# Kernel optimization log

Hardware: AMD Instinct MI355X
Metric: run time of the kernel (lower is better)

## Reference

```python
import jax, jax.numpy as jnp
import numpy as np

B, S, D, H = 2, 2048, 1024, 16
DK = D // H
NEG = -1.0e9


def setup_inputs() -> dict:
    key = jax.random.key(0)
    ks = jax.random.split(key, 11)
    inp = {
        "q": jax.random.normal(ks[0], (B, S, D), jnp.float32),
        "k": jax.random.normal(ks[1], (B, S, D), jnp.float32),
        "v": jax.random.normal(ks[2], (B, S, D), jnp.float32),
        "mask": jnp.tril(jnp.ones((S, S), jnp.int32))[None, None],  # causal [1,1,S,S]
    }
    scale = 0.02
    inp["w_q"] = jax.random.normal(ks[3], (D, D), jnp.float32) * scale
    inp["b_q"] = jnp.zeros((D,), jnp.float32)
    inp["w_k"] = jax.random.normal(ks[4], (D, D), jnp.float32) * scale
    inp["b_k"] = jnp.zeros((D,), jnp.float32)
    inp["w_v"] = jax.random.normal(ks[5], (D, D), jnp.float32) * scale
    inp["b_v"] = jnp.zeros((D,), jnp.float32)
    inp["w_o"] = jax.random.normal(ks[6], (D, D), jnp.float32) * scale
    inp["b_o"] = jnp.zeros((D,), jnp.float32)
    return inp


def reference(q, k, v, mask, w_q, b_q, w_k, b_k, w_v, b_v, w_o, b_o):
    # projections: [B,S,D] -> [B,H,S,DK]
    def proj(x, w, b):
        y = jnp.einsum("bsd,de->bse", x, w) + b
        return y.reshape(B, S, H, DK).transpose(0, 2, 1, 3)

    Q = proj(q, w_q, b_q)
    K = proj(k, w_k, b_k)
    V = proj(v, w_v, b_v)
    # explicit scores matrix, faithful to the original naive attention
    scores = jnp.einsum("bhsd,bhtd->bhst", Q, K) / jnp.sqrt(jnp.float32(DK))
    scores = jnp.where(mask == 0, NEG, scores)
    attn = jax.nn.softmax(scores, axis=-1)  # dropout p=0.0 -> identity
    x = jnp.einsum("bhst,bhtd->bhsd", attn, V)
    x = x.transpose(0, 2, 1, 3).reshape(B, S, D)
    return jnp.einsum("bsd,de->bse", x, w_o) + b_o
```

## Files before the change

kernel.cpp:

```cpp
#include <hip/hip_runtime.h>
#include <hip/hip_bf16.h>

typedef __bf16 bf16;
typedef __bf16 bf16x2 __attribute__((ext_vector_type(2)));
typedef __bf16 bf16x8 __attribute__((ext_vector_type(8)));
typedef float f32x4 __attribute__((ext_vector_type(4)));

#define MFMA16(a, b, c) __builtin_amdgcn_mfma_f32_16x16x32_bf16(a, b, c, 0, 0, 0)

#define QSCALE 0.18033688f

#define GLOAD_LDS(g, l)                                              \
  __builtin_amdgcn_global_load_lds(                                  \
      (const __attribute__((address_space(1))) void*)(g),            \
      (__attribute__((address_space(3))) void*)(l), 16, 0, 0)

__global__ __launch_bounds__(256) void convert_k(const float* __restrict__ q,
                                                 const float* __restrict__ k,
                                                 const float* __restrict__ v,
                                                 bf16* __restrict__ qb,
                                                 bf16* __restrict__ kb,
                                                 bf16* __restrict__ vb) {
  const float* src = blockIdx.y == 0 ? q : blockIdx.y == 1 ? k : v;
  bf16* dst = blockIdx.y == 0 ? qb : blockIdx.y == 1 ? kb : vb;
  const size_t i = ((size_t)blockIdx.x * 256 + threadIdx.x) * 8;
  float4 a = *(const float4*)(src + i);
  float4 b = *(const float4*)(src + i + 4);
  bf16x8 o;
  o[0] = (bf16)a.x; o[1] = (bf16)a.y; o[2] = (bf16)a.z; o[3] = (bf16)a.w;
  o[4] = (bf16)b.x; o[5] = (bf16)b.y; o[6] = (bf16)b.z; o[7] = (bf16)b.w;
  *(bf16x8*)(dst + i) = o;
}

__global__ __launch_bounds__(256) void transpose_w(const float* __restrict__ w0,
                                                   const float* __restrict__ w1,
                                                   const float* __restrict__ w2,
                                                   const float* __restrict__ w3,
                                                   bf16* __restrict__ dst) {
  __shared__ bf16 T[64][68];
  const float* W = blockIdx.z == 0 ? w0 : blockIdx.z == 1 ? w1
                   : blockIdx.z == 2 ? w2 : w3;
  bf16* Y = dst + (size_t)blockIdx.z * 1024 * 1024;
  const int t = threadIdx.x, r = t >> 2, c4 = t & 3;
  const int k0 = blockIdx.y * 64, n0 = blockIdx.x * 64;

  const float4* src = (const float4*)(W + (size_t)(k0 + r) * 1024 + n0 + c4 * 16);
  float4 f0 = src[0], f1 = src[1], f2 = src[2], f3 = src[3];
  bf16* row = &T[r][c4 * 16];
  row[0] = (bf16)f0.x; row[1] = (bf16)f0.y; row[2] = (bf16)f0.z; row[3] = (bf16)f0.w;
  row[4] = (bf16)f1.x; row[5] = (bf16)f1.y; row[6] = (bf16)f1.z; row[7] = (bf16)f1.w;
  row[8] = (bf16)f2.x; row[9] = (bf16)f2.y; row[10] = (bf16)f2.z; row[11] = (bf16)f2.w;
  row[12] = (bf16)f3.x; row[13] = (bf16)f3.y; row[14] = (bf16)f3.z; row[15] = (bf16)f3.w;
  __syncthreads();

  bf16x8 o0, o1;
#pragma unroll
  for (int j = 0; j < 8; ++j) o0[j] = T[c4 * 16 + j][r];
#pragma unroll
  for (int j = 0; j < 8; ++j) o1[j] = T[c4 * 16 + 8 + j][r];
  bf16* d = Y + (size_t)(n0 + r) * 1024 + k0 + c4 * 16;
  *(bf16x8*)d = o0;
  *(bf16x8*)(d + 8) = o1;
}

template <int QKV, int MT>
__global__ __launch_bounds__(256) void gemm128(
    const bf16* __restrict__ xq, const bf16* __restrict__ xk,
    const bf16* __restrict__ xv, const bf16* __restrict__ Wt,
    const float* __restrict__ bq, const float* __restrict__ bk,
    const float* __restrict__ bv, bf16* __restrict__ Qp,
    bf16* __restrict__ Kp, bf16* __restrict__ Vtp, float* __restrict__ Yf) {
  __shared__ bf16 Al[MT * 32 * 32];
  __shared__ bf16 Bl[128 * 32];

  const int z = QKV ? blockIdx.z : 0;
  const bf16* X = QKV ? (z == 0 ? xq : z == 1 ? xk : xv) : xq;
  const bf16* Bt = Wt + (size_t)z * 1048576;
  const float* bias = QKV ? (z == 0 ? bq : z == 1 ? bk : bv) : bq;
  const float escale = (QKV && z == 0) ? QSCALE : 1.0f;

  const int t = threadIdx.x;
  const int wave = t >> 6, lane = t & 63, quad = lane >> 4, l16 = lane & 15;
  const int wm = (wave >> 1) * (MT * 16), wn = (wave & 1) * 64;
  const int bm = blockIdx.y * (MT * 32), bn = blockIdx.x * 128;

  const int off = wave * 1024 + lane * 16;
  const int srow = off >> 6;
  const int scol = (off & 63) >> 1;
  const bf16* gA0 = X + (size_t)(bm + srow) * 1024 + scol;
  const bf16* gA1 = X + (size_t)(bm + 64 + srow) * 1024 + scol;
  const bf16* gB0 = Bt + (size_t)(bn + srow) * 1024 + scol;
  const bf16* gB1 = Bt + (size_t)(bn + 64 + srow) * 1024 + scol;
  bf16* ldsA0 = Al + wave * 512;
  bf16* ldsA1 = Al + 2048 + wave * 512;
  bf16* ldsB0 = Bl + wave * 512;
  bf16* ldsB1 = Bl + 2048 + wave * 512;

  f32x4 acc[MT][4] = {};

  for (int kb = 0; kb < 1024; kb += 32) {
    GLOAD_LDS(gA0 + kb, ldsA0);
    if (MT == 4) GLOAD_LDS(gA1 + kb, ldsA1);
    GLOAD_LDS(gB0 + kb, ldsB0);
    GLOAD_LDS(gB1 + kb, ldsB1);
    __syncthreads();

    bf16x8 af[MT], bfr[4];
#pragma unroll
    for (int mt = 0; mt < MT; ++mt)
      af[mt] = *(const bf16x8*)(Al + (wm + mt * 16 + l16) * 32 + quad * 8);
#pragma unroll
    for (int nt = 0; nt < 4; ++nt)
      bfr[nt] = *(const bf16x8*)(Bl + (wn + nt * 16 + l16) * 32 + quad * 8);
#pragma unroll
    for (int mt = 0; mt < MT; ++mt)
#pragma unroll
      for (int nt = 0; nt < 4; ++nt)
        acc[mt][nt] = MFMA16(af[mt], bfr[nt], acc[mt][nt]);
    __syncthreads();
  }

  if (QKV && z == 2) {
    __shared__ bf16 Tt[64 * 136];
    const int b = bm >> 11;
#pragma unroll
    for (int half = 0; half < 2; ++half) {
      if ((wave & 1) == half) {
#pragma unroll
        for (int nt = 0; nt < 4; ++nt) {
          const int ln = nt * 16 + l16;
          const float bia = bias[bn + half * 64 + ln];
#pragma unroll
          for (int mt = 0; mt < 4; ++mt)
#pragma unroll
            for (int r = 0; r < 4; ++r) {
              const int m = wm + mt * 16 + quad * 4 + r;
              Tt[ln * 136 + m] = (bf16)(acc[mt][nt][r] + bia);
            }
        }
      }
      __syncthreads();
      {
        const int ln = t >> 2, seg = (t & 3) * 32;
        const int gn = bn + half * 64 + ln;
        const int h = gn >> 6, dk = gn & 63;
        const int s0 = (bm & 2047) + seg;
        bf16* dst = Vtp + ((size_t)(b * 16 + h) * 64 + dk) * 2048 + s0;
        const bf16* srcp = Tt + ln * 136 + seg;
#pragma unroll
        for (int j = 0; j < 4; ++j)
          *(bf16x8*)(dst + j * 8) = *(const bf16x8*)(srcp + j * 8);
      }
      __syncthreads();
    }
  } else {
#pragma unroll
    for (int mt = 0; mt < MT; ++mt)
#pragma unroll
      for (int nt = 0; nt < 4; ++nt) {
        const int gn = bn + wn + nt * 16 + l16;
        const float bia = bias[gn];
#pragma unroll
        for (int r = 0; r < 4; ++r) {
          const int gm = bm + wm + mt * 16 + quad * 4 + r;
          const float val = (acc[mt][nt][r] + bia) * escale;
          if (!QKV) {
            Yf[(size_t)gm * 1024 + gn] = val;
          } else {
            const int b = gm >> 11, s = gm & 2047;
            const int h = gn >> 6, dk = gn & 63;
            bf16* Y = (z == 0) ? Qp : Kp;
            Y[((size_t)(b * 16 + h) * 2048 + s) * 64 + dk] = (bf16)val;
          }
        }
      }
  }
}

__global__ __launch_bounds__(256) void attn_k(const bf16* __restrict__ Q,
                                              const bf16* __restrict__ K,
                                              const bf16* __restrict__ Vt,
                                              bf16* __restrict__ X) {
  __shared__ bf16 Kl[64 * 72];
  __shared__ bf16 Vl[64 * 72];
  __shared__ bf16 Pb[4][16 * 72];

  const int t = threadIdx.x;
  const int wave = t >> 6, lane = t & 63, quad = lane >> 4, l16 = lane & 15;
  const int pairx = blockIdx.x, bh = blockIdx.y;
  const int b = bh >> 4, h = bh & 15;

  const bf16* Qb = Q + (size_t)bh * 2048 * 64;
  const bf16* Kb = K + (size_t)bh * 2048 * 64;
  const bf16* Vb = Vt + (size_t)bh * 64 * 2048;

  const int srow = t >> 2;
  const int scol = (t & 3) * 16;

  bf16x8 onesf;
#pragma unroll
  for (int i = 0; i < 8; ++i) onesf[i] = (bf16)1.0f;

  bf16* Pw = Pb[wave];

  for (int phase = 0; phase < 2; ++phase) {
    const int qtile = phase ? (31 - pairx) : pairx;
    const int ntiles = qtile + 1;
    const int q0 = qtile * 64 + wave * 16;

    bf16x8 qf0 = *(const bf16x8*)(Qb + (q0 + l16) * 64 + quad * 8);
    bf16x8 qf1 = *(const bf16x8*)(Qb + (q0 + l16) * 64 + 32 + quad * 8);

    f32x4 o[4] = {};
    f32x4 o4 = {};

    {
      const bf16* kp = Kb + srow * 64 + scol;
      const bf16* vp = Vb + (size_t)srow * 2048 + scol;
      bf16x8 k0r = *(const bf16x8*)kp;
      bf16x8 k1r = *(const bf16x8*)(kp + 8);
      bf16x8 v0r = *(const bf16x8*)vp;
      bf16x8 v1r = *(const bf16x8*)(vp + 8);
      *(bf16x8*)(Kl + srow * 72 + scol) = k0r;
      *(bf16x8*)(Kl + srow * 72 + scol + 8) = k1r;
      *(bf16x8*)(Vl + srow * 72 + scol) = v0r;
      *(bf16x8*)(Vl + srow * 72 + scol + 8) = v1r;
    }
    __syncthreads();

    for (int kt = 0; kt < ntiles; ++kt) {
      const int k0 = kt * 64;
      const bool more = (kt + 1) < ntiles;
      bf16x8 kr0, kr1, vr0, vr1;
      if (more) {
        const bf16* kp = Kb + (k0 + 64 + srow) * 64 + scol;
        const bf16* vp = Vb + (size_t)srow * 2048 + k0 + 64 + scol;
        kr0 = *(const bf16x8*)kp;
        kr1 = *(const bf16x8*)(kp + 8);
        vr0 = *(const bf16x8*)vp;
        vr1 = *(const bf16x8*)(vp + 8);
      }

      f32x4 sc[4];
#pragma unroll
      for (int nt = 0; nt < 4; ++nt) {
        bf16x8 kf0 = *(const bf16x8*)(Kl + (nt * 16 + l16) * 72 + quad * 8);
        bf16x8 kf1 = *(const bf16x8*)(Kl + (nt * 16 + l16) * 72 + 32 + quad * 8);
        f32x4 s = {};
        s = MFMA16(qf0, kf0, s);
        s = MFMA16(qf1, kf1, s);
        sc[nt] = s;
      }

#pragma unroll
      for (int r = 0; r < 4; ++r) {
        const int row = quad * 4 + r;
        const int qg = q0 + row;
#pragma unroll
        for (int nt = 0; nt < 4; ++nt) {
          const int key = k0 + nt * 16 + l16;
          const float p = (key <= qg) ? exp2f(sc[nt][r]) : 0.f;
          Pw[row * 72 + nt * 16 + l16] = (bf16)p;
        }
      }
      __builtin_amdgcn_s_waitcnt(0xC07F);

      bf16x8 pf0 = *(const bf16x8*)(Pw + l16 * 72 + quad * 8);
      bf16x8 pf1 = *(const bf16x8*)(Pw + l16 * 72 + 32 + quad * 8);
      o4 = MFMA16(pf0, onesf, o4);
      o4 = MFMA16(pf1, onesf, o4);
#pragma unroll
      for (int dt = 0; dt < 4; ++dt) {
        bf16x8 vf0 = *(const bf16x8*)(Vl + (dt * 16 + l16) * 72 + quad * 8);
        bf16x8 vf1 = *(const bf16x8*)(Vl + (dt * 16 + l16) * 72 + 32 + quad * 8);
        o[dt] = MFMA16(pf0, vf0, o[dt]);
        o[dt] = MFMA16(pf1, vf1, o[dt]);
      }

      __syncthreads();
      if (more) {
        *(bf16x8*)(Kl + srow * 72 + scol) = kr0;
        *(bf16x8*)(Kl + srow * 72 + scol + 8) = kr1;
        *(bf16x8*)(Vl + srow * 72 + scol) = vr0;
        *(bf16x8*)(Vl + srow * 72 + scol + 8) = vr1;
        __syncthreads();
      }
    }

#pragma unroll
    for (int r = 0; r < 4; ++r) {
      const float rinv = 1.0f / o4[r];
      const int qg = q0 + quad * 4 + r;
#pragma unroll
      for (int dt = 0; dt < 4; ++dt) {
        const int col = h * 64 + dt * 16 + l16;
        X[((size_t)b * 2048 + qg) * 1024 + col] = (bf16)(o[dt][r] * rinv);
      }
    }
    __syncthreads();
  }
}

extern "C" void kernel_launch(void* const* d_in, const int* in_sizes, int n_in,
                              void* d_out, int out_size, void* d_ws,
                              size_t ws_size, hipStream_t stream) {
  const float* q = (const float*)d_in[0];
  const float* k = (const float*)d_in[1];
  const float* v = (const float*)d_in[2];
  const float* w_q = (const float*)d_in[4];
  const float* b_q = (const float*)d_in[5];
  const float* w_k = (const float*)d_in[6];
  const float* b_k = (const float*)d_in[7];
  const float* w_v = (const float*)d_in[8];
  const float* b_v = (const float*)d_in[9];
  const float* w_o = (const float*)d_in[10];
  const float* b_o = (const float*)d_in[11];

  bf16* ws = (bf16*)d_ws;
  const size_t NELEM = (size_t)4096 * 1024;
  bf16* Qp = ws;
  bf16* Kp = ws + NELEM;
  bf16* Vtp = ws + 2 * NELEM;
  bf16* Xp = ws + 3 * NELEM;
  bf16* Wt = ws + 4 * NELEM;
  bf16* Wto = Wt + 3145728;
  bf16* qb = Xp;
  bf16* kb = (bf16*)d_out;
  bf16* vb = kb + NELEM;

  convert_k<<<dim3(2048, 3), 256, 0, stream>>>(q, k, v, qb, kb, vb);
  transpose_w<<<dim3(16, 16, 4), 256, 0, stream>>>(w_q, w_k, w_v, w_o, Wt);

  gemm128<1, 4><<<dim3(8, 32, 3), 256, 0, stream>>>(
      qb, kb, vb, Wt, b_q, b_k, b_v, Qp, Kp, Vtp, nullptr);
  attn_k<<<dim3(16, 32), 256, 0, stream>>>(Qp, Kp, Vtp, Xp);
  gemm128<0, 2><<<dim3(8, 64), 256, 0, stream>>>(
      Xp, nullptr, nullptr, Wto, b_o, nullptr, nullptr, nullptr, nullptr,
      nullptr, (float*)d_out);
}
```

Measured before the change: 261.0 us.

## Register-prefetch GEMM with padded LDS, permute K rows and skip interior masks

The projection GEMMs drop direct global-to-LDS loads in favour of register prefetching of the next 64-wide K slab into padded LDS tiles, which halves barrier count per K and overlaps loads with MFMA work. They also set an occupancy hint and reuse the A tile buffer for the V transpose. In attention, K rows are permuted in LDS so each lane's scores map to adjacent keys, enabling packed bf16x2 stores of P, and the causal mask check is skipped for fully interior tiles. The changes risk higher register pressure and depend on the permutation matching the P/V layout.

```diff
diff --git a/kernel.cpp b/kernel.cpp
--- a/kernel.cpp
+++ b/kernel.cpp
@@ -9,11 +9,6 @@
 #define MFMA16(a, b, c) __builtin_amdgcn_mfma_f32_16x16x32_bf16(a, b, c, 0, 0, 0)
 
 #define QSCALE 0.18033688f
-
-#define GLOAD_LDS(g, l)                                              \
-  __builtin_amdgcn_global_load_lds(                                  \
-      (const __attribute__((address_space(1))) void*)(g),            \
-      (__attribute__((address_space(3))) void*)(l), 16, 0, 0)
 
 __global__ __launch_bounds__(256) void convert_k(const float* __restrict__ q,
                                                  const float* __restrict__ k,
@@ -64,14 +59,15 @@
 }
 
 template <int QKV, int MT>
-__global__ __launch_bounds__(256) void gemm128(
+__global__ __launch_bounds__(256, 3) void gemm_p(
     const bf16* __restrict__ xq, const bf16* __restrict__ xk,
     const bf16* __restrict__ xv, const bf16* __restrict__ Wt,
     const float* __restrict__ bq, const float* __restrict__ bk,
     const float* __restrict__ bv, bf16* __restrict__ Qp,
     bf16* __restrict__ Kp, bf16* __restrict__ Vtp, float* __restrict__ Yf) {
-  __shared__ bf16 Al[MT * 32 * 32];
-  __shared__ bf16 Bl[128 * 32];
+  constexpr int AROWS = MT * 32;
+  __shared__ bf16 Al[AROWS * 72];
+  __shared__ bf16 Bl[128 * 72];
 
   const int z = QKV ? blockIdx.z : 0;
   const bf16* X = QKV ? (z == 0 ? xq : z == 1 ? xk : xv) : xq;
@@ -82,47 +78,65 @@
   const int t = threadIdx.x;
   const int wave = t >> 6, lane = t & 63, quad = lane >> 4, l16 = lane & 15;
   const int wm = (wave >> 1) * (MT * 16), wn = (wave & 1) * 64;
-  const int bm = blockIdx.y * (MT * 32), bn = blockIdx.x * 128;
-
-  const int off = wave * 1024 + lane * 16;
-  const int srow = off >> 6;
-  const int scol = (off & 63) >> 1;
-  const bf16* gA0 = X + (size_t)(bm + srow) * 1024 + scol;
-  const bf16* gA1 = X + (size_t)(bm + 64 + srow) * 1024 + scol;
-  const bf16* gB0 = Bt + (size_t)(bn + srow) * 1024 + scol;
-  const bf16* gB1 = Bt + (size_t)(bn + 64 + srow) * 1024 + scol;
-  bf16* ldsA0 = Al + wave * 512;
-  bf16* ldsA1 = Al + 2048 + wave * 512;
-  bf16* ldsB0 = Bl + wave * 512;
-  bf16* ldsB1 = Bl + 2048 + wave * 512;
+  const int bm = blockIdx.y * AROWS, bn = blockIdx.x * 128;
+
+  constexpr int NA = (MT == 4) ? 4 : 2;
+  const int arow = (MT == 4) ? (t >> 1) : (t >> 2);
+  const int acol = (MT == 4) ? ((t & 1) * 32) : ((t & 3) * 16);
+  const int brow = t >> 1, bcol = (t & 1) * 32;
+  const bf16* gA = X + (size_t)(bm + arow) * 1024 + acol;
+  const bf16* gB = Bt + (size_t)(bn + brow) * 1024 + bcol;
+
+  bf16x8 ra[NA], rb[4];
+#pragma unroll
+  for (int j = 0; j < NA; ++j) ra[j] = *(const bf16x8*)(gA + j * 8);
+#pragma unroll
+  for (int j = 0; j < 4; ++j) rb[j] = *(const bf16x8*)(gB + j * 8);
 
   f32x4 acc[MT][4] = {};
 
-  for (int kb = 0; kb < 1024; kb += 32) {
-    GLOAD_LDS(gA0 + kb, ldsA0);
-    if (MT == 4) GLOAD_LDS(gA1 + kb, ldsA1);
-    GLOAD_LDS(gB0 + kb, ldsB0);
-    GLOAD_LDS(gB1 + kb, ldsB1);
-    __syncthreads();
-
-    bf16x8 af[MT], bfr[4];
-#pragma unroll
-    for (int mt = 0; mt < MT; ++mt)
-      af[mt] = *(const bf16x8*)(Al + (wm + mt * 16 + l16) * 32 + quad * 8);
-#pragma unroll
-    for (int nt = 0; nt < 4; ++nt)
-      bfr[nt] = *(const bf16x8*)(Bl + (wn + nt * 16 + l16) * 32 + quad * 8);
-#pragma unroll
-    for (int mt = 0; mt < MT; ++mt)
+  for (int kb = 0; kb < 1024; kb += 64) {
+    __syncthreads();
+#pragma unroll
+    for (int j = 0; j < NA; ++j)
+      *(bf16x8*)(Al + arow * 72 + acol + j * 8) = ra[j];
+#pragma unroll
+    for (int j = 0; j < 4; ++j)
+      *(bf16x8*)(Bl + brow * 72 + bcol + j * 8) = rb[j];
+    __syncthreads();
+
+    if (kb + 64 < 1024) {
+#pragma unroll
+      for (int j = 0; j < NA; ++j)
+        ra[j] = *(const bf16x8*)(gA + kb + 64 + j * 8);
+#pragma unroll
+      for (int j = 0; j < 4; ++j)
+        rb[j] = *(const bf16x8*)(gB + kb + 64 + j * 8);
+    }
+
+#pragma unroll
+    for (int kk = 0; kk < 2; ++kk) {
+      bf16x8 af[MT], bfr[4];
+#pragma unroll
+      for (int mt = 0; mt < MT; ++mt)
+        af[mt] =
+            *(const bf16x8*)(Al + (wm + mt * 16 + l16) * 72 + kk * 32 + quad * 8);
 #pragma unroll
       for (int nt = 0; nt < 4; ++nt)
-        acc[mt][nt] = MFMA16(af[mt], bfr[nt], acc[mt][nt]);
-    __syncthreads();
+        bfr[nt] =
+            *(const bf16x8*)(Bl + (wn + nt * 16 + l16) * 72 + kk * 32 + quad * 8);
+#pragma unroll
+      for (int mt = 0; mt < MT; ++mt)
+#pragma unroll
+        for (int nt = 0; nt < 4; ++nt)
+          acc[mt][nt] = MFMA16(af[mt], bfr[nt], acc[mt][nt]);
+    }
   }
 
   if (QKV && z == 2) {
-    __shared__ bf16 Tt[64 * 136];
+    bf16* Tt = Al;
     const int b = bm >> 11;
+    __syncthreads();
 #pragma unroll
     for (int half = 0; half < 2; ++half) {
       if ((wave & 1) == half) {
@@ -145,11 +159,11 @@
         const int gn = bn + half * 64 + ln;
         const int h = gn >> 6, dk = gn & 63;
         const int s0 = (bm & 2047) + seg;
-        bf16* dst = Vtp + ((size_t)(b * 16 + h) * 64 + dk) * 2048 + s0;
+        bf16* dstp = Vtp + ((size_t)(b * 16 + h) * 64 + dk) * 2048 + s0;
         const bf16* srcp = Tt + ln * 136 + seg;
 #pragma unroll
         for (int j = 0; j < 4; ++j)
-          *(bf16x8*)(dst + j * 8) = *(const bf16x8*)(srcp + j * 8);
+          *(bf16x8*)(dstp + j * 8) = *(const bf16x8*)(srcp + j * 8);
       }
       __syncthreads();
     }
@@ -196,6 +210,7 @@
 
   const int srow = t >> 2;
   const int scol = (t & 3) * 16;
+  const int crow = (srow & 32) + ((srow & 1) << 4) + ((srow & 31) >> 1);
 
   bf16x8 onesf;
 #pragma unroll
@@ -221,8 +236,8 @@
       bf16x8 k1r = *(const bf16x8*)(kp + 8);
       bf16x8 v0r = *(const bf16x8*)vp;
       bf16x8 v1r = *(const bf16x8*)(vp + 8);
-      *(bf16x8*)(Kl + srow * 72 + scol) = k0r;
-      *(bf16x8*)(Kl + srow * 72 + scol + 8) = k1r;
+      *(bf16x8*)(Kl + crow * 72 + scol) = k0r;
+      *(bf16x8*)(Kl + crow * 72 + scol + 8) = k1r;
       *(bf16x8*)(Vl + srow * 72 + scol) = v0r;
       *(bf16x8*)(Vl + srow * 72 + scol + 8) = v1r;
     }
@@ -252,16 +267,27 @@
         sc[nt] = s;
       }
 
+      const bool interior = (k0 + 63) <= q0;
 #pragma unroll
       for (int r = 0; r < 4; ++r) {
         const int row = quad * 4 + r;
-        const int qg = q0 + row;
-#pragma unroll
-        for (int nt = 0; nt < 4; ++nt) {
-          const int key = k0 + nt * 16 + l16;
-          const float p = (key <= qg) ? exp2f(sc[nt][r]) : 0.f;
-          Pw[row * 72 + nt * 16 + l16] = (bf16)p;
+        float e0 = exp2f(sc[0][r]);
+        float e1 = exp2f(sc[1][r]);
+        float e2 = exp2f(sc[2][r]);
+        float e3 = exp2f(sc[3][r]);
+        if (!interior) {
+          const int qg = q0 + row;
+          const int key0 = k0 + 2 * l16;
+          if (key0 > qg) e0 = 0.f;
+          if (key0 + 1 > qg) e1 = 0.f;
+          if (key0 + 32 > qg) e2 = 0.f;
+          if (key0 + 33 > qg) e3 = 0.f;
         }
+        bf16x2 p01, p23;
+        p01[0] = (bf16)e0; p01[1] = (bf16)e1;
+        p23[0] = (bf16)e2; p23[1] = (bf16)e3;
+        *(bf16x2*)(Pw + row * 72 + 2 * l16) = p01;
+        *(bf16x2*)(Pw + row * 72 + 32 + 2 * l16) = p23;
       }
       __builtin_amdgcn_s_waitcnt(0xC07F);
 
@@ -279,8 +305,8 @@
 
       __syncthreads();
       if (more) {
-        *(bf16x8*)(Kl + srow * 72 + scol) = kr0;
-        *(bf16x8*)(Kl + srow * 72 + scol + 8) = kr1;
+        *(bf16x8*)(Kl + crow * 72 + scol) = kr0;
+        *(bf16x8*)(Kl + crow * 72 + scol + 8) = kr1;
         *(bf16x8*)(Vl + srow * 72 + scol) = vr0;
         *(bf16x8*)(Vl + srow * 72 + scol + 8) = vr1;
         __syncthreads();
@@ -331,10 +357,10 @@
   convert_k<<<dim3(2048, 3), 256, 0, stream>>>(q, k, v, qb, kb, vb);
   transpose_w<<<dim3(16, 16, 4), 256, 0, stream>>>(w_q, w_k, w_v, w_o, Wt);
 
-  gemm128<1, 4><<<dim3(8, 32, 3), 256, 0, stream>>>(
+  gemm_p<1, 4><<<dim3(8, 32, 3), 256, 0, stream>>>(
       qb, kb, vb, Wt, b_q, b_k, b_v, Qp, Kp, Vtp, nullptr);
   attn_k<<<dim3(16, 32), 256, 0, stream>>>(Qp, Kp, Vtp, Xp);
-  gemm128<0, 2><<<dim3(8, 64), 256, 0, stream>>>(
+  gemm_p<0, 2><<<dim3(8, 64), 256, 0, stream>>>(
       Xp, nullptr, nullptr, Wto, b_o, nullptr, nullptr, nullptr, nullptr,
       nullptr, (float*)d_out);
 }
```

New measurement: 243.9 us. -6.5%, faster.
